# Kernel optimization log

Hardware: AMD Instinct MI355X
Metric: run time of the kernel (lower is better)

Reference implementation:

```python
import jax, jax.numpy as jnp
import numpy as np

B, T, V, C = 4, 2048, 1024, 256
NB_L, NB_M, NB_H = 16, 32, 64


def _band_w(basis, coeffs, soft):
    # basis: (V, 2*nb), coeffs: (C, 2*nb) -> w: (V, C)
    w = basis @ coeffs.T
    return jax.nn.softmax(w, axis=0) if soft else w


def _rms_norm(x):
    eps = jnp.asarray(jnp.finfo(x.dtype).eps, x.dtype)
    return x * jax.lax.rsqrt(jnp.mean(jnp.square(x), axis=-1, keepdims=True) + eps)


def _retrieve(x, basis, qc, kc, vc, decay_logit):
    # x: (B,T,V) -> (B,T,C); decay-weighted dense T x T retrieval
    q = x @ _band_w(basis, qc, True)
    k = x @ _band_w(basis, kc, True)
    v = x @ _band_w(basis, vc, True)
    scores = jnp.einsum('btc,bsc->bts', q, k)
    decay = jax.nn.sigmoid(decay_logit)
    pos = jnp.arange(T)
    diff = pos[None, :] - pos[:, None]  # diff[i,j] = j - i (as in torch code)
    dw = (decay ** jnp.maximum(diff - 1, 0).astype(x.dtype)) * (diff > 0).astype(x.dtype)
    return jnp.einsum('bts,bsc->btc', scores * dw[None], v)


def _project(r, basis, oc, out_scale):
    return jnp.einsum('btc,vc->btv', r, basis @ oc.T) * out_scale


def _transform(x, basis, read_c, mix, bias):
    z = x @ _band_w(basis, read_c, True)
    return jax.nn.gelu(z @ mix + bias, approximate=False)


def _write_back(h, basis, write_c, out_scale):
    return jnp.einsum('btc,vc->btv', h, basis @ write_c.T) * out_scale


def setup_inputs() -> dict:
    key = jax.random.key(0)
    ks = iter(jax.random.split(key, 48))
    s = 0.02

    def rn(shape, scale=s):
        return jax.random.normal(next(ks), shape, dtype=jnp.float32) * scale

    d = {
        'x': jax.random.normal(next(ks), (B, T, V), dtype=jnp.float32),
        'basis_low': jax.random.normal(next(ks), (V, 2 * NB_L), dtype=jnp.float32),
        'basis_mid': jax.random.normal(next(ks), (V, 2 * NB_M), dtype=jnp.float32),
        'basis_high': jax.random.normal(next(ks), (V, 2 * NB_H), dtype=jnp.float32),
    }
    for pre, nb, dec in (('slow', NB_L, 4.0), ('fast', NB_H, 2.0)):
        for nm in ('q', 'k', 'v', 'o'):
            d[f'{pre}_{nm}'] = rn((C, 2 * nb))
        d[f'{pre}_decay'] = jnp.asarray(dec, jnp.float32)
        d[f'{pre}_scale'] = jnp.asarray(0.1, jnp.float32)
    for pre, nb in (('low', NB_L), ('mid', NB_M), ('high', NB_H)):
        d[f'{pre}_read'] = rn((C, 2 * nb))
        d[f'{pre}_write'] = rn((C, 2 * nb))
        d[f'{pre}_mix'] = rn((C, C))
        d[f'{pre}_bias'] = jnp.zeros((C,), jnp.float32)
        d[f'{pre}_oscale'] = jnp.asarray(0.1, jnp.float32)
    d['tg_w'] = rn((C, C)); d['tg_b'] = jnp.zeros((C,), jnp.float32)
    d['alpha_w'] = rn((C, C)); d['alpha_b'] = jnp.zeros((C,), jnp.float32)
    for nm in ('mem_slow_scale', 'mem_fast_scale', 'op_low_scale', 'op_mid_scale', 'op_high_scale'):
        d[nm] = jnp.ones((1,), jnp.float32)
    return d


def reference(x, basis_low, basis_mid, basis_high,
              slow_q, slow_k, slow_v, slow_o, slow_decay, slow_scale,
              fast_q, fast_k, fast_v, fast_o, fast_decay, fast_scale,
              low_read, low_write, low_mix, low_bias, low_oscale,
              mid_read, mid_write, mid_mix, mid_bias, mid_oscale,
              high_read, high_write, high_mix, high_bias, high_oscale,
              tg_w, tg_b, alpha_w, alpha_b,
              mem_slow_scale, mem_fast_scale, op_low_scale, op_mid_scale, op_high_scale):
    # Phase 1: temporal mixing
    xn = _rms_norm(x)
    r_slow = _retrieve(xn, basis_low, slow_q, slow_k, slow_v, slow_decay)
    r_fast = _retrieve(xn, basis_high, fast_q, fast_k, fast_v, fast_decay)
    tg = jax.nn.sigmoid(r_slow @ tg_w + tg_b)
    r_fast = tg * r_fast
    x = x + (_project(r_slow, basis_low, slow_o, slow_scale) * mem_slow_scale
             + _project(r_fast, basis_high, fast_o, fast_scale) * mem_fast_scale)
    # Phase 2: band processing
    xn = _rms_norm(x)
    h_low = _transform(xn, basis_low, low_read, low_mix, low_bias)
    h_mid = _transform(xn, basis_mid, mid_read, mid_mix, mid_bias)
    h_high = _transform(xn, basis_high, high_read, high_mix, high_bias)
    ag = jax.nn.sigmoid(h_low @ alpha_w + alpha_b)
    h_high = ag * h_high
    x = x + (_write_back(h_low, basis_low, low_write, low_oscale) * op_low_scale
             + _write_back(h_mid, basis_mid, mid_write, mid_oscale) * op_mid_scale
             + _write_back(h_high, basis_high, high_write, high_oscale) * op_high_scale)
    return x
```

## Files before the change

kernel.cpp:

```cpp
#include <hip/hip_runtime.h>
#include <math.h>

#define BB 4
#define TT 2048
#define VV 1024
#define CC 256
#define MR (BB*TT)

using short8  = __attribute__((ext_vector_type(8))) short;
using ushort8 = __attribute__((ext_vector_type(8))) unsigned short;
using f32x4   = __attribute__((ext_vector_type(4))) float;

__device__ __forceinline__ float bs2f(unsigned short s) {
    return __uint_as_float(((unsigned int)s) << 16);
}
__device__ __forceinline__ unsigned short f2bs(float f) {
    unsigned int u = __float_as_uint(f);
    u += 0x7fffu + ((u >> 16) & 1u);
    return (unsigned short)(u >> 16);
}
__device__ __forceinline__ void gl_lds16(const void* g, void* l) {
    __builtin_amdgcn_global_load_lds(
        (const __attribute__((address_space(1))) unsigned int*)g,
        (__attribute__((address_space(3))) unsigned int*)l, 16, 0, 0);
}
__device__ __forceinline__ float sigm(float x) { return 1.f / (1.f + expf(-x)); }

struct CastJob { const float* src; unsigned short* dst; int n; };
struct CastArgs { CastJob j[17]; };

__global__ void cast_bf16_multi(CastArgs a) {
    CastJob jb = a.j[blockIdx.x];
    int off = (blockIdx.y * 256 + threadIdx.x) * 8;
    if (off + 8 > jb.n) return;
    float4 v0 = *reinterpret_cast<const float4*>(jb.src + off);
    float4 v1 = *reinterpret_cast<const float4*>(jb.src + off + 4);
    ushort8 u;
    u[0] = f2bs(v0.x); u[1] = f2bs(v0.y); u[2] = f2bs(v0.z); u[3] = f2bs(v0.w);
    u[4] = f2bs(v1.x); u[5] = f2bs(v1.y); u[6] = f2bs(v1.z); u[7] = f2bs(v1.w);
    *reinterpret_cast<ushort8*>(jb.dst + off) = u;
}

__global__ void softmax_rows(unsigned short* __restrict__ w) {
    int r = blockIdx.x, t = threadIdx.x;
    unsigned short* row = w + (size_t)r * 1024;
    ushort4 u = reinterpret_cast<ushort4*>(row)[t];
    float v0 = bs2f(u.x), v1 = bs2f(u.y), v2 = bs2f(u.z), v3 = bs2f(u.w);
    __shared__ float red[256];
    red[t] = fmaxf(fmaxf(v0, v1), fmaxf(v2, v3));
    __syncthreads();
    for (int o = 128; o > 0; o >>= 1) { if (t < o) red[t] = fmaxf(red[t], red[t + o]); __syncthreads(); }
    float mx = red[0]; __syncthreads();
    float e0 = expf(v0 - mx), e1 = expf(v1 - mx), e2 = expf(v2 - mx), e3 = expf(v3 - mx);
    red[t] = e0 + e1 + e2 + e3;
    __syncthreads();
    for (int o = 128; o > 0; o >>= 1) { if (t < o) red[t] += red[t + o]; __syncthreads(); }
    float inv = 1.f / red[0];
    ushort4 o4;
    o4.x = f2bs(e0 * inv); o4.y = f2bs(e1 * inv); o4.z = f2bs(e2 * inv); o4.w = f2bs(e3 * inv);
    reinterpret_cast<ushort4*>(row)[t] = o4;
}

__global__ void prep_T5(const float* s0, const float* s1, const float* s2,
                        const float* s3, const float* s4,
                        unsigned short* d0, unsigned short* d1, unsigned short* d2,
                        unsigned short* d3, unsigned short* d4) {
    int y = blockIdx.y;
    const float* W = y == 0 ? s0 : y == 1 ? s1 : y == 2 ? s2 : y == 3 ? s3 : s4;
    unsigned short* WT = y == 0 ? d0 : y == 1 ? d1 : y == 2 ? d2 : y == 3 ? d3 : d4;
    int n = blockIdx.x, k = threadIdx.x;
    WT[(size_t)n * 256 + k] = f2bs(W[(size_t)k * 256 + n]);
}

__global__ void rmsnorm_k(const float* __restrict__ x, unsigned short* __restrict__ xn) {
    int row = blockIdx.x, t = threadIdx.x;
    const float4 v = reinterpret_cast<const float4*>(x + (size_t)row * VV)[t];
    __shared__ float red[256];
    red[t] = v.x * v.x + v.y * v.y + v.z * v.z + v.w * v.w;
    __syncthreads();
    for (int o = 128; o > 0; o >>= 1) { if (t < o) red[t] += red[t + o]; __syncthreads(); }
    float r = rsqrtf(red[0] * (1.f / VV) + 1.1920929e-7f);
    ushort4 u;
    u.x = f2bs(v.x * r); u.y = f2bs(v.y * r); u.z = f2bs(v.z * r); u.w = f2bs(v.w * r);
    reinterpret_cast<ushort4*>(xn + (size_t)row * VV)[t] = u;
}

__global__ void transpose4_k(const unsigned short* __restrict__ qkv,
                             unsigned short* __restrict__ vt_s,
                             unsigned short* __restrict__ vt_f,
                             unsigned short* __restrict__ kts_s,
                             unsigned short* __restrict__ kts_f,
                             const float* __restrict__ dls,
                             const float* __restrict__ dlf) {
    __shared__ unsigned short tile[32][33];
    int z = blockIdx.z, b = z & 3, which = z >> 2;
    int srcoff = which == 0 ? 512 : which == 1 ? 1280 : which == 2 ? 256 : 1024;
    unsigned short* dst = which == 0 ? vt_s : which == 1 ? vt_f : which == 2 ? kts_s : kts_f;
    float l2d = 0.f;
    if (which == 2) l2d = log2f(sigm(dls[0]));
    if (which == 3) l2d = log2f(sigm(dlf[0]));
    int t0 = blockIdx.x * 32, c0 = blockIdx.y * 32;
    int tx = threadIdx.x & 31, ty = threadIdx.x >> 5;
    const unsigned short* src = qkv + srcoff;
    #pragma unroll
    for (int i = 0; i < 4; ++i) {
        int r = ty + i * 8;
        tile[r][tx] = src[(size_t)(b * TT + t0 + r) * 1536 + c0 + tx];
    }
    __syncthreads();
    float w = (which >= 2) ? exp2f(l2d * (float)((t0 + tx) & 127)) : 1.f;
    #pragma unroll
    for (int i = 0; i < 4; ++i) {
        int r = ty + i * 8;
        dst[((size_t)b * CC + c0 + r) * TT + t0 + tx] = f2bs(bs2f(tile[tx][r]) * w);
    }
}

__device__ __forceinline__ void gemm64_core(
    const unsigned short* A, int lda, const unsigned short* Bt, int ldb,
    int K, int m0, int n0, short8* As, short8* Bs, f32x4 (&acc)[2][2]) {
    const int tid = threadIdx.x;
    const int lane = tid & 63, wid = tid >> 6;
    const int wm = wid >> 1, wn = wid & 1;
    const int lrow = tid >> 2, lch = tid & 3;
    const int sws = lch ^ ((lrow >> 1) & 3);
    const unsigned short* ag = A + (size_t)(m0 + lrow) * lda + lch * 8;
    const unsigned short* bg = Bt + (size_t)(n0 + lrow) * ldb + lch * 8;
    #pragma unroll
    for (int i = 0; i < 2; ++i)
        #pragma unroll
        for (int j = 0; j < 2; ++j) acc[i][j] = {0.f, 0.f, 0.f, 0.f};
    const int g = lane >> 4;
    const int ra0 = wm * 32 + (lane & 15);
    const int rb0 = wn * 32 + (lane & 15);
    for (int k0 = 0; k0 < K; k0 += 32) {
        As[lrow * 4 + sws] = *reinterpret_cast<const short8*>(ag + k0);
        Bs[lrow * 4 + sws] = *reinterpret_cast<const short8*>(bg + k0);
        __syncthreads();
        short8 af[2], bf[2];
        #pragma unroll
        for (int i = 0; i < 2; ++i) {
            int ra = ra0 + i * 16;
            af[i] = As[ra * 4 + (g ^ ((ra >> 1) & 3))];
            int rb = rb0 + i * 16;
            bf[i] = Bs[rb * 4 + (g ^ ((rb >> 1) & 3))];
        }
        #pragma unroll
        for (int i = 0; i < 2; ++i)
            #pragma unroll
            for (int j = 0; j < 2; ++j)
                acc[i][j] = __builtin_amdgcn_mfma_f32_16x16x32_bf16(af[i], bf[j], acc[i][j], 0, 0, 0);
        __syncthreads();
    }
}

#define EPI_LOOP(MV, NV, VV_, BODY)                                            \
    {   const int lane_ = threadIdx.x & 63, wid_ = threadIdx.x >> 6;           \
        const int wm_ = wid_ >> 1, wn_ = wid_ & 1;                             \
        _Pragma("unroll")                                                      \
        for (int i_ = 0; i_ < 2; ++i_)                                         \
        { _Pragma("unroll")                                                    \
          for (int j_ = 0; j_ < 2; ++j_)                                       \
          { _Pragma("unroll")                                                  \
            for (int r_ = 0; r_ < 4; ++r_)                                     \
            { int MV = m0 + wm_ * 32 + i_ * 16 + (lane_ >> 4) * 4 + r_;        \
              int NV = n0 + wn_ * 32 + j_ * 16 + (lane_ & 15);                 \
              float VV_ = acc[i_][j_][r_];                                     \
              BODY } } } }

struct MJob {
    const unsigned short* A; const unsigned short* Bt; unsigned short* outb;
    const float* s1; const float* s2;
    int lda, ldb, K, ldo, gx, nblk;
};
struct MJobs5 { MJob j[5]; };

template<int EPI>
__global__ __launch_bounds__(256)
void gemm_multi_k(MJobs5 js) {
    int bid = blockIdx.x, ji = 0, base = 0;
    while (bid >= base + js.j[ji].nblk) { base += js.j[ji].nblk; ++ji; }
    MJob jb = js.j[ji];
    int rem = bid - base;
    int m0 = (rem / jb.gx) * 64, n0 = (rem % jb.gx) * 64;
    __shared__ short8 As[256], Bs[256];
    f32x4 acc[2][2];
    gemm64_core(jb.A, jb.lda, jb.Bt, jb.ldb, jb.K, m0, n0, As, Bs, acc);
    float sc = 1.f;
    if constexpr (EPI == 4) sc = jb.s1[0] * jb.s2[0];
    EPI_LOOP(m, n, v, { jb.outb[(size_t)m * jb.ldo + n] = f2bs(v * sc); })
}

__global__ __launch_bounds__(256)
void sig_k(const unsigned short* A, int lda, const unsigned short* Bt,
           const float* bias, const unsigned short* aux, int ldaux,
           unsigned short* outb, int ldo, int coloff) {
    int m0 = blockIdx.y * 64, n0 = blockIdx.x * 64;
    __shared__ short8 As[256], Bs[256];
    f32x4 acc[2][2];
    gemm64_core(A, lda, Bt, 256, 256, m0, n0, As, Bs, acc);
    EPI_LOOP(m, n, v, {
        float s = sigm(v + bias[n]);
        float a = bs2f(aux[(size_t)m * ldaux + n]);
        outb[(size_t)m * ldo + coloff + n] = f2bs(s * a);
    })
}

__global__ __launch_bounds__(256)
void gelu3_k(const unsigned short* zbuf, const unsigned short* WT_mix,
             const float* lb, const float* mb, const float* hb,
             unsigned short* hcat, unsigned short* hhigh) {
    int zi = blockIdx.z;
    const unsigned short* A = zbuf + zi * 256;
    const unsigned short* Bt = WT_mix + (size_t)zi * 65536;
    const float* bias = zi == 0 ? lb : zi == 1 ? mb : hb;
    unsigned short* outb = zi == 2 ? hhigh : hcat;
    int ldo = zi == 2 ? 256 : 768;
    int coloff = zi == 1 ? 256 : 0;
    int m0 = blockIdx.y * 64, n0 = blockIdx.x * 64;
    __shared__ short8 As[256], Bs[256];
    f32x4 acc[2][2];
    gemm64_core(A, 768, Bt, 256, 256, m0, n0, As, Bs, acc);
    EPI_LOOP(m, n, v, {
        float z = v + bias[n];
        float h = 0.5f * z * (1.f + erff(z * 0.70710678118654752f));
        outb[(size_t)m * ldo + coloff + n] = f2bs(h);
    })
}

__global__ __launch_bounds__(256)
void gstate_k(const unsigned short* kts_s, const unsigned short* vt_s,
              const unsigned short* kts_f, const unsigned short* vt_f,
              float* Gs, float* Gf) {
    int zz = blockIdx.z;
    int sel = zz >> 6, z2 = zz & 63;
    int zb = z2 >> 4, zp = z2 & 15;
    const unsigned short* A  = (sel ? kts_f : kts_s) + (size_t)(zb * CC) * TT + zp * 128;
    const unsigned short* Bt = (sel ? vt_f  : vt_s)  + (size_t)(zb * CC) * TT + zp * 128;
    float* G = (sel ? Gf : Gs) + (size_t)z2 * 65536;
    int m0 = blockIdx.y * 64, n0 = blockIdx.x * 64;
    __shared__ short8 As[256], Bs[256];
    f32x4 acc[2][2];
    gemm64_core(A, TT, Bt, TT, 128, m0, n0, As, Bs, acc);
    EPI_LOOP(m, n, v, { G[(size_t)m * 256 + n] = v; })
}

__global__ __launch_bounds__(256)
void inter_k(const unsigned short* qkv,
             const unsigned short* ST_s, const unsigned short* ST_f,
             const float* dls, const float* dlf,
             unsigned short* rcat, unsigned short* rfast) {
    int zz = blockIdx.z;
    int sel = zz >= 60, z2 = sel ? zz - 60 : zz;
    int zb = z2 / 15, zp = z2 % 15;
    const unsigned short* A = qkv + (sel ? 768 : 0) + (size_t)(zb * TT + zp * 128) * 1536;
    const unsigned short* Bt = (sel ? ST_f : ST_s) + (size_t)z2 * 65536;
    unsigned short* outb = sel ? rfast : rcat;
    int ldo = sel ? 256 : 512;
    float l2d = log2f(sigm(sel ? dlf[0] : dls[0]));
    int m0 = blockIdx.y * 64, n0 = blockIdx.x * 64;
    __shared__ short8 As[256], Bs[256];
    f32x4 acc[2][2];
    gemm64_core(A, 1536, Bt, 256, 256, m0, n0, As, Bs, acc);
    EPI_LOOP(m, n, v, {
        float rs = exp2f(l2d * (float)(127 - m));
        size_t idx = (size_t)(zb * TT + zp * 128 + m) * ldo + n;
        outb[idx] = f2bs(bs2f(outb[idx]) + v * rs);
    })
}

struct EpiP {
    float* outf; const float* addf;
    unsigned short* outb; int ldo;
};

template<int EPI>
__global__ __launch_bounds__(256)
void gemm128_k(const unsigned short* __restrict__ A, int lda,
               const unsigned short* __restrict__ Bt, int ldb, int K, EpiP ep) {
    __shared__ short8 As[1024], Bs[1024];
    const int tid = threadIdx.x;
    const int lane = tid & 63, wid = tid >> 6;
    const int wm = wid >> 1, wn = wid & 1;

    int lin = blockIdx.y * gridDim.x + blockIdx.x;
    int ngw = gridDim.x * gridDim.y;
    int q8 = ngw >> 3;
    int sw = (lin & 7) * q8 + (lin >> 3);
    const int m0 = (sw / gridDim.x) * 128, n0 = (sw % gridDim.x) * 128;

    const int srow = lane >> 3, schk = (lane & 7) ^ srow;
    const unsigned short* ga = A + (size_t)(m0 + wid * 32 + srow) * lda + schk * 8;
    const unsigned short* gb = Bt + (size_t)(n0 + wid * 32 + srow) * ldb + schk * 8;
    short8* lA = &As[(wid * 32) * 8];
    short8* lB = &Bs[(wid * 32) * 8];

    const int fr = lane & 15, fg = lane >> 4;

    f32x4 acc[4][4];
    #pragma unroll
    for (int i = 0; i < 4; ++i)
        #pragma unroll
        for (int j = 0; j < 4; ++j) acc[i][j] = {0.f, 0.f, 0.f, 0.f};

    for (int k0 = 0; k0 < K; k0 += 64) {
        #pragma unroll
        for (int q = 0; q < 4; ++q) {
            gl_lds16(ga + (size_t)(q * 8) * lda + k0, lA + q * 64);
            gl_lds16(gb + (size_t)(q * 8) * ldb + k0, lB + q * 64);
        }
        __syncthreads();
        #pragma unroll
        for (int kk = 0; kk < 2; ++kk) {
            short8 af[4], bf[4];
            #pragma unroll
            for (int i = 0; i < 4; ++i) {
                int ra = wm * 64 + i * 16 + fr;
                af[i] = As[ra * 8 + ((kk * 4 + fg) ^ (ra & 7))];
                int rb = wn * 64 + i * 16 + fr;
                bf[i] = Bs[rb * 8 + ((kk * 4 + fg) ^ (rb & 7))];
            }
            #pragma unroll
            for (int i = 0; i < 4; ++i)
                #pragma unroll
                for (int j = 0; j < 4; ++j)
                    acc[i][j] = __builtin_amdgcn_mfma_f32_16x16x32_bf16(af[i], bf[j], acc[i][j], 0, 0, 0);
        }
        __syncthreads();
    }

    #pragma unroll
    for (int i = 0; i < 4; ++i) {
        #pragma unroll
        for (int j = 0; j < 4; ++j) {
            #pragma unroll
            for (int r = 0; r < 4; ++r) {
                int m = m0 + wm * 64 + i * 16 + fg * 4 + r;
                int n = n0 + wn * 64 + j * 16 + fr;
                float v = acc[i][j][r];
                if constexpr (EPI == 0) {
                    ep.outb[(size_t)m * ep.ldo + n] = f2bs(v);
                } else {
                    size_t idx = (size_t)m * ep.ldo + n;
                    ep.outf[idx] = ep.addf[idx] + v;
                }
            }
        }
    }
}

__global__ __launch_bounds__(256)
void attn_k(const unsigned short* __restrict__ qkv,
            const unsigned short* __restrict__ vt_s,
            const unsigned short* __restrict__ vt_f,
            const float* __restrict__ dls, const float* __restrict__ dlf,
            unsigned short* __restrict__ rcat, unsigned short* __restrict__ rfast) {
    int y = blockIdx.y;
    int qoff = y ? 768 : 0, koff = y ? 1024 : 256;
    const unsigned short* vt = y ? vt_f : vt_s;
    unsigned short* rout = y ? rfast : rcat;
    int ldr = y ? 256 : 512;
    float l2d = log2f(sigm(y ? dlf[0] : dls[0]));

    int blk = blockIdx.x;
    int b = blk >> 7;
    int t0 = (blk & 127) << 4;
    int tid = threadIdx.x;
    int lane = tid & 63, wid = tid >> 6;

    __shared__ short8 Pl[4][64];
    __shared__ float  red[16][260];

    short8 qf[8];
    const size_t rowq = (size_t)(b * TT + t0 + (lane & 15)) * 1536 + qoff + (lane >> 4) * 8;
    #pragma unroll
    for (int ch = 0; ch < 8; ++ch)
        qf[ch] = *reinterpret_cast<const short8*>(qkv + rowq + ch * 32);

    f32x4 racc[16];
    #pragma unroll
    for (int i = 0; i < 16; ++i) racc[i] = {0.f, 0.f, 0.f, 0.f};

    unsigned short* pb = reinterpret_cast<unsigned short*>(&Pl[wid][0]);

    int sBeg = t0 & ~31;
    int sEnd = (t0 & ~127) + 128;
    const int tl = (lane >> 4) * 4;

    for (int s0 = sBeg + wid * 32; s0 < sEnd; s0 += 128) {
        #pragma unroll
        for (int h = 0; h < 2; ++h) {
            f32x4 sacc = {0.f, 0.f, 0.f, 0.f};
            const unsigned short* kb =
                qkv + (size_t)(b * TT + s0 + h * 16 + (lane & 15)) * 1536 + koff + (lane >> 4) * 8;
            #pragma unroll
            for (int ch = 0; ch < 8; ++ch) {
                short8 kf = *reinterpret_cast<const short8*>(kb + ch * 32);
                sacc = __builtin_amdgcn_mfma_f32_16x16x32_bf16(qf[ch], kf, sacc, 0, 0, 0);
            }
            int scol = s0 + h * 16 + (lane & 15);
            #pragma unroll
            for (int r = 0; r < 4; ++r) {
                int trow = t0 + tl + r;
                int d = scol - trow;
                float w = (d > 0) ? exp2f(l2d * (float)(d - 1)) : 0.f;
                int prow = tl + r, pcol = h * 16 + (lane & 15);
                int swp = (pcol >> 3) ^ ((prow >> 1) & 3);
                pb[(prow * 4 + swp) * 8 + (pcol & 7)] = f2bs(sacc[r] * w);
            }
        }
        asm volatile("s_waitcnt lgkmcnt(0)" ::: "memory");
        __builtin_amdgcn_sched_barrier(0);
        short8 pf;
        { int prow = lane & 15; pf = Pl[wid][prow * 4 + ((lane >> 4) ^ ((prow >> 1) & 3))]; }
        const unsigned short* vb = vt + ((size_t)b * CC + (lane & 15)) * TT + s0 + (lane >> 4) * 8;
        #pragma unroll
        for (int nt = 0; nt < 16; ++nt) {
            short8 vf = *reinterpret_cast<const short8*>(vb + (size_t)nt * 16 * TT);
            racc[nt] = __builtin_amdgcn_mfma_f32_16x16x32_bf16(pf, vf, racc[nt], 0, 0, 0);
        }
    }

    for (int w = 0; w < 4; ++w) {
        if (wid == w) {
            #pragma unroll
            for (int nt = 0; nt < 16; ++nt)
                #pragma unroll
                for (int r = 0; r < 4; ++r) {
                    int row = tl + r, col = nt * 16 + (lane & 15);
                    if (w == 0) red[row][col] = racc[nt][r];
                    else        red[row][col] += racc[nt][r];
                }
        }
        __syncthreads();
    }

    {
        int row = tid >> 4, c0 = (tid & 15) * 16;
        ushort8 lo, hi;
        #pragma unroll
        for (int j = 0; j < 8; ++j) lo[j] = f2bs(red[row][c0 + j]);
        #pragma unroll
        for (int j = 0; j < 8; ++j) hi[j] = f2bs(red[row][c0 + 8 + j]);
        unsigned short* dst = rout + (size_t)(b * TT + t0 + row) * ldr + c0;
        *reinterpret_cast<ushort8*>(dst)     = lo;
        *reinterpret_cast<ushort8*>(dst + 8) = hi;
    }
}

__global__ void scan_states(const float* __restrict__ G,
                            const float* __restrict__ dlogit,
                            unsigned short* __restrict__ ST) {
    int b = blockIdx.y;
    int e0 = (blockIdx.x * 256 + threadIdx.x) * 4;
    float d = sigm(dlogit[0]);
    float dL = exp2f(log2f(d) * 128.f);
    float4 s = {0.f, 0.f, 0.f, 0.f};
    int i = e0 >> 8, j0 = e0 & 255;
    for (int c = 15; c >= 1; --c) {
        float4 g = *reinterpret_cast<const float4*>(G + (((size_t)(b * 16 + c)) << 16) + e0);
        s.x = g.x + dL * s.x; s.y = g.y + dL * s.y;
        s.z = g.z + dL * s.z; s.w = g.w + dL * s.w;
        unsigned short* dst = ST + (((size_t)(b * 15 + c - 1)) << 16);
        dst[(j0 + 0) * 256 + i] = f2bs(s.x);
        dst[(j0 + 1) * 256 + i] = f2bs(s.y);
        dst[(j0 + 2) * 256 + i] = f2bs(s.z);
        dst[(j0 + 3) * 256 + i] = f2bs(s.w);
    }
}

extern "C" void kernel_launch(void* const* d_in, const int* in_sizes, int n_in,
                              void* d_out, int out_size, void* d_ws, size_t ws_size,
                              hipStream_t stream) {
    (void)in_sizes; (void)n_in; (void)out_size; (void)ws_size;
    const float* x          = (const float*)d_in[0];
    const float* basis_low  = (const float*)d_in[1];
    const float* basis_mid  = (const float*)d_in[2];
    const float* basis_high = (const float*)d_in[3];
    const float* slow_q = (const float*)d_in[4];
    const float* slow_k = (const float*)d_in[5];
    const float* slow_v = (const float*)d_in[6];
    const float* slow_o = (const float*)d_in[7];
    const float* slow_decay = (const float*)d_in[8];
    const float* slow_scale = (const float*)d_in[9];
    const float* fast_q = (const float*)d_in[10];
    const float* fast_k = (const float*)d_in[11];
    const float* fast_v = (const float*)d_in[12];
    const float* fast_o = (const float*)d_in[13];
    const float* fast_decay = (const float*)d_in[14];
    const float* fast_scale = (const float*)d_in[15];
    const float* low_read  = (const float*)d_in[16];
    const float* low_write = (const float*)d_in[17];
    const float* low_mix   = (const float*)d_in[18];
    const float* low_bias  = (const float*)d_in[19];
    const float* low_oscale= (const float*)d_in[20];
    const float* mid_read  = (const float*)d_in[21];
    const float* mid_write = (const float*)d_in[22];
    const float* mid_mix   = (const float*)d_in[23];
    const float* mid_bias  = (const float*)d_in[24];
    const float* mid_oscale= (const float*)d_in[25];
    const float* high_read  = (const float*)d_in[26];
    const float* high_write = (const float*)d_in[27];
    const float* high_mix   = (const float*)d_in[28];
    const float* high_bias  = (const float*)d_in[29];
    const float* high_oscale= (const float*)d_in[30];
    const float* tg_w    = (const float*)d_in[31];
    const float* tg_b    = (const float*)d_in[32];
    const float* alpha_w = (const float*)d_in[33];
    const float* alpha_b = (const float*)d_in[34];
    const float* mem_slow_scale = (const float*)d_in[35];
    const float* mem_fast_scale = (const float*)d_in[36];
    const float* op_low_scale   = (const float*)d_in[37];
    const float* op_mid_scale   = (const float*)d_in[38];
    const float* op_high_scale  = (const float*)d_in[39];
    float* out = (float*)d_out;

    char* ws = (char*)d_ws;
    size_t off = 0;
    auto alloc = [&](size_t n) { char* p = ws + off; off += (n + 255) & ~(size_t)255; return p; };
    unsigned short* WT_p1   = (unsigned short*)alloc((size_t)6 * CC * VV * 2);
    unsigned short* WT_read = (unsigned short*)alloc((size_t)3 * CC * VV * 2);
    unsigned short* Wcat_o  = (unsigned short*)alloc((size_t)VV * 512 * 2);
    unsigned short* Wcat_w  = (unsigned short*)alloc((size_t)VV * 768 * 2);
    unsigned short* WT_mix  = (unsigned short*)alloc((size_t)3 * 65536 * 2);
    unsigned short* WT_tg   = (unsigned short*)alloc((size_t)65536 * 2);
    unsigned short* WT_al   = (unsigned short*)alloc((size_t)65536 * 2);
    unsigned short* bb_low  = (unsigned short*)alloc((size_t)VV * 32 * 2);
    unsigned short* bb_mid  = (unsigned short*)alloc((size_t)VV * 64 * 2);
    unsigned short* bb_high = (unsigned short*)alloc((size_t)VV * 128 * 2);
    unsigned short* cqkv_l  = (unsigned short*)alloc((size_t)768 * 32 * 2);
    unsigned short* cqkv_h  = (unsigned short*)alloc((size_t)768 * 128 * 2);
    unsigned short* crd_l   = (unsigned short*)alloc((size_t)256 * 32 * 2);
    unsigned short* crd_m   = (unsigned short*)alloc((size_t)256 * 64 * 2);
    unsigned short* crd_h   = (unsigned short*)alloc((size_t)256 * 128 * 2);
    unsigned short* cO_s    = (unsigned short*)alloc((size_t)256 * 32 * 2);
    unsigned short* cO_f    = (unsigned short*)alloc((size_t)256 * 128 * 2);
    unsigned short* cW_l    = (unsigned short*)alloc((size_t)256 * 32 * 2);
    unsigned short* cW_m    = (unsigned short*)alloc((size_t)256 * 64 * 2);
    unsigned short* cW_h    = (unsigned short*)alloc((size_t)256 * 128 * 2);
    unsigned short* xn      = (unsigned short*)alloc((size_t)MR * VV * 2);
    unsigned short* qkv     = (unsigned short*)alloc((size_t)MR * 1536 * 2);
    unsigned short* vt_s    = (unsigned short*)alloc((size_t)BB * CC * TT * 2);
    unsigned short* vt_f    = (unsigned short*)alloc((size_t)BB * CC * TT * 2);
    unsigned short* kts_s   = (unsigned short*)alloc((size_t)BB * CC * TT * 2);
    unsigned short* kts_f   = (unsigned short*)alloc((size_t)BB * CC * TT * 2);
    unsigned short* ST_s    = (unsigned short*)alloc((size_t)BB * 15 * 65536 * 2);
    unsigned short* ST_f    = (unsigned short*)alloc((size_t)BB * 15 * 65536 * 2);
    unsigned short* rcat    = (unsigned short*)alloc((size_t)MR * 512 * 2);
    unsigned short* rfast   = (unsigned short*)alloc((size_t)MR * CC * 2);
    unsigned short* hhigh   = (unsigned short*)alloc((size_t)MR * CC * 2);
    float* Gs = (float*)xn;
    float* Gf = (float*)rcat;
    unsigned short* z    = qkv;
    unsigned short* hcat = qkv + (size_t)MR * 768;

    {
        CastArgs ca;
        int i = 0;
        auto J = [&](const float* s, unsigned short* d, int n) { ca.j[i].src = s; ca.j[i].dst = d; ca.j[i].n = n; ++i; };
        J(basis_low,  bb_low,  VV * 32);
        J(basis_mid,  bb_mid,  VV * 64);
        J(basis_high, bb_high, VV * 128);
        J(slow_q, cqkv_l + 0 * 256 * 32, 256 * 32);
        J(slow_k, cqkv_l + 1 * 256 * 32, 256 * 32);
        J(slow_v, cqkv_l + 2 * 256 * 32, 256 * 32);
        J(fast_q, cqkv_h + 0 * 256 * 128, 256 * 128);
        J(fast_k, cqkv_h + 1 * 256 * 128, 256 * 128);
        J(fast_v, cqkv_h + 2 * 256 * 128, 256 * 128);
        J(low_read,  crd_l, 256 * 32);
        J(mid_read,  crd_m, 256 * 64);
        J(high_read, crd_h, 256 * 128);
        J(slow_o,    cO_s,  256 * 32);
        J(fast_o,    cO_f,  256 * 128);
        J(low_write, cW_l,  256 * 32);
        J(mid_write, cW_m,  256 * 64);
        J(high_write,cW_h,  256 * 128);
        cast_bf16_multi<<<dim3(17, 64), 256, 0, stream>>>(ca);
    }

    {
        MJobs5 js;
        auto S = [&](int i, const unsigned short* A, int lda, const unsigned short* B, int K,
                     unsigned short* o, int nb) {
            js.j[i].A = A; js.j[i].Bt = B; js.j[i].outb = o; js.j[i].s1 = nullptr; js.j[i].s2 = nullptr;
            js.j[i].lda = lda; js.j[i].ldb = K; js.j[i].K = K; js.j[i].ldo = VV; js.j[i].gx = 16; js.j[i].nblk = nb;
        };
        S(0, cqkv_l, 32,  bb_low,  32,  WT_p1,                    192);
        S(1, cqkv_h, 128, bb_high, 128, WT_p1 + (size_t)768 * VV, 192);
        S(2, crd_l,  32,  bb_low,  32,  WT_read,                   64);
        S(3, crd_m,  64,  bb_mid,  64,  WT_read + (size_t)256 * VV, 64);
        S(4, crd_h,  128, bb_high, 128, WT_read + (size_t)512 * VV, 64);
        gemm_multi_k<0><<<576, 256, 0, stream>>>(js);
    }
    softmax_rows<<<2304, 256, 0, stream>>>(WT_p1);

    {
        MJobs5 js;
        auto S = [&](int i, const unsigned short* A, int lda, const unsigned short* B, int K,
                     unsigned short* o, int ldo, const float* s1, const float* s2) {
            js.j[i].A = A; js.j[i].Bt = B; js.j[i].outb = o; js.j[i].s1 = s1; js.j[i].s2 = s2;
            js.j[i].lda = lda; js.j[i].ldb = K; js.j[i].K = K; js.j[i].ldo = ldo; js.j[i].gx = 4; js.j[i].nblk = 64;
        };
        S(0, bb_low,  32,  cO_s, 32,  Wcat_o,       512, slow_scale,  mem_slow_scale);
        S(1, bb_high, 128, cO_f, 128, Wcat_o + 256, 512, fast_scale,  mem_fast_scale);
        S(2, bb_low,  32,  cW_l, 32,  Wcat_w,       768, low_oscale,  op_low_scale);
        S(3, bb_mid,  64,  cW_m, 64,  Wcat_w + 256, 768, mid_oscale,  op_mid_scale);
        S(4, bb_high, 128, cW_h, 128, Wcat_w + 512, 768, high_oscale, op_high_scale);
        gemm_multi_k<4><<<320, 256, 0, stream>>>(js);
    }

    prep_T5<<<dim3(256, 5), 256, 0, stream>>>(tg_w, alpha_w, low_mix, mid_mix, high_mix,
                                              WT_tg, WT_al, WT_mix, WT_mix + 65536, WT_mix + 131072);

    rmsnorm_k<<<MR, 256, 0, stream>>>(x, xn);
    { EpiP ep{}; ep.outb = qkv; ep.ldo = 1536;
      gemm128_k<0><<<dim3(12, 64), 256, 0, stream>>>(xn, 1024, WT_p1, 1024, 1024, ep); }
    transpose4_k<<<dim3(64, 8, 16), 256, 0, stream>>>(qkv, vt_s, vt_f, kts_s, kts_f, slow_decay, fast_decay);
    gstate_k<<<dim3(4, 4, 128), 256, 0, stream>>>(kts_s, vt_s, kts_f, vt_f, Gs, Gf);
    scan_states<<<dim3(64, 4), 256, 0, stream>>>(Gs, slow_decay, ST_s);
    scan_states<<<dim3(64, 4), 256, 0, stream>>>(Gf, fast_decay, ST_f);
    attn_k<<<dim3(512, 2), 256, 0, stream>>>(qkv, vt_s, vt_f, slow_decay, fast_decay, rcat, rfast);
    inter_k<<<dim3(4, 2, 120), 256, 0, stream>>>(qkv, ST_s, ST_f, slow_decay, fast_decay, rcat, rfast);
    sig_k<<<dim3(4, 128), 256, 0, stream>>>(rcat, 512, WT_tg, tg_b, rfast, 256, rcat, 512, 256);
    { EpiP ep{}; ep.outf = out; ep.addf = x; ep.ldo = 1024;
      gemm128_k<3><<<dim3(8, 64), 256, 0, stream>>>(rcat, 512, Wcat_o, 512, 512, ep); }

    rmsnorm_k<<<MR, 256, 0, stream>>>(out, xn);
    { EpiP ep{}; ep.outb = z; ep.ldo = 768;
      gemm128_k<0><<<dim3(6, 64), 256, 0, stream>>>(xn, 1024, WT_read, 1024, 1024, ep); }
    gelu3_k<<<dim3(4, 128, 3), 256, 0, stream>>>(z, WT_mix, low_bias, mid_bias, high_bias, hcat, hhigh);
    sig_k<<<dim3(4, 128), 256, 0, stream>>>(hcat, 768, WT_al, alpha_b, hhigh, 256, hcat, 768, 512);
    { EpiP ep{}; ep.outf = out; ep.addf = out; ep.ldo = 1024;
      gemm128_k<3><<<dim3(6, 64), 256, 0, stream>>>(hcat, 768, Wcat_w, 768, 768, ep); }
}
```

Baseline: 315.3 us.

## Double-buffer LDS in gemm128_k and merge the two scan_states launches

The 128x128 GEMM kernel now keeps two LDS buffers and issues the global-to-LDS loads for the next K tile before computing the current one. It waits with explicit vmcnt counts and raw s_barrier instead of a full __syncthreads, so load latency can overlap MFMA work. The two scan_states launches for the slow and fast paths are merged into one launch using blockIdx.z, saving one kernel launch. The GEMM doubles its LDS footprint, which may lower occupancy, and its correctness depends on the hand-written waitcnt matching the eight outstanding loads per stage.

```diff
diff --git a/kernel.cpp b/kernel.cpp
--- a/kernel.cpp
+++ b/kernel.cpp
@@ -278,7 +278,7 @@
 __global__ __launch_bounds__(256)
 void gemm128_k(const unsigned short* __restrict__ A, int lda,
                const unsigned short* __restrict__ Bt, int ldb, int K, EpiP ep) {
-    __shared__ short8 As[1024], Bs[1024];
+    __shared__ short8 As[2][1024], Bs[2][1024];
     const int tid = threadIdx.x;
     const int lane = tid & 63, wid = tid >> 6;
     const int wm = wid >> 1, wn = wid & 1;
@@ -292,8 +292,6 @@
     const int srow = lane >> 3, schk = (lane & 7) ^ srow;
     const unsigned short* ga = A + (size_t)(m0 + wid * 32 + srow) * lda + schk * 8;
     const unsigned short* gb = Bt + (size_t)(n0 + wid * 32 + srow) * ldb + schk * 8;
-    short8* lA = &As[(wid * 32) * 8];
-    short8* lB = &Bs[(wid * 32) * 8];
 
     const int fr = lane & 15, fg = lane >> 4;
 
@@ -303,22 +301,36 @@
         #pragma unroll
         for (int j = 0; j < 4; ++j) acc[i][j] = {0.f, 0.f, 0.f, 0.f};
 
-    for (int k0 = 0; k0 < K; k0 += 64) {
+    auto stage = [&](int buf, int k0) {
+        short8* lA = &As[buf][(wid * 32) * 8];
+        short8* lB = &Bs[buf][(wid * 32) * 8];
         #pragma unroll
         for (int q = 0; q < 4; ++q) {
             gl_lds16(ga + (size_t)(q * 8) * lda + k0, lA + q * 64);
             gl_lds16(gb + (size_t)(q * 8) * ldb + k0, lB + q * 64);
         }
-        __syncthreads();
+    };
+
+    stage(0, 0);
+    int cur = 0;
+    for (int k0 = 0; k0 < K; k0 += 64) {
+        if (k0 + 64 < K) {
+            stage(cur ^ 1, k0 + 64);
+            asm volatile("s_waitcnt vmcnt(8)" ::: "memory");
+        } else {
+            asm volatile("s_waitcnt vmcnt(0)" ::: "memory");
+        }
+        __builtin_amdgcn_s_barrier();
+        __builtin_amdgcn_sched_barrier(0);
         #pragma unroll
         for (int kk = 0; kk < 2; ++kk) {
             short8 af[4], bf[4];
             #pragma unroll
             for (int i = 0; i < 4; ++i) {
                 int ra = wm * 64 + i * 16 + fr;
-                af[i] = As[ra * 8 + ((kk * 4 + fg) ^ (ra & 7))];
+                af[i] = As[cur][ra * 8 + ((kk * 4 + fg) ^ (ra & 7))];
                 int rb = wn * 64 + i * 16 + fr;
-                bf[i] = Bs[rb * 8 + ((kk * 4 + fg) ^ (rb & 7))];
+                bf[i] = Bs[cur][rb * 8 + ((kk * 4 + fg) ^ (rb & 7))];
             }
             #pragma unroll
             for (int i = 0; i < 4; ++i)
@@ -326,7 +338,9 @@
                 for (int j = 0; j < 4; ++j)
                     acc[i][j] = __builtin_amdgcn_mfma_f32_16x16x32_bf16(af[i], bf[j], acc[i][j], 0, 0, 0);
         }
-        __syncthreads();
+        __builtin_amdgcn_sched_barrier(0);
+        __builtin_amdgcn_s_barrier();
+        cur ^= 1;
     }
 
     #pragma unroll
@@ -448,12 +462,15 @@
     }
 }
 
-__global__ void scan_states(const float* __restrict__ G,
-                            const float* __restrict__ dlogit,
-                            unsigned short* __restrict__ ST) {
+__global__ void scan_states2(const float* __restrict__ Gs, const float* __restrict__ Gf,
+                             const float* __restrict__ dls, const float* __restrict__ dlf,
+                             unsigned short* __restrict__ STs, unsigned short* __restrict__ STf) {
+    int sel = blockIdx.z;
+    const float* G = sel ? Gf : Gs;
+    unsigned short* ST = sel ? STf : STs;
+    float d = sigm(sel ? dlf[0] : dls[0]);
     int b = blockIdx.y;
     int e0 = (blockIdx.x * 256 + threadIdx.x) * 4;
-    float d = sigm(dlogit[0]);
     float dL = exp2f(log2f(d) * 128.f);
     float4 s = {0.f, 0.f, 0.f, 0.f};
     int i = e0 >> 8, j0 = e0 & 255;
@@ -617,8 +634,7 @@
       gemm128_k<0><<<dim3(12, 64), 256, 0, stream>>>(xn, 1024, WT_p1, 1024, 1024, ep); }
     transpose4_k<<<dim3(64, 8, 16), 256, 0, stream>>>(qkv, vt_s, vt_f, kts_s, kts_f, slow_decay, fast_decay);
     gstate_k<<<dim3(4, 4, 128), 256, 0, stream>>>(kts_s, vt_s, kts_f, vt_f, Gs, Gf);
-    scan_states<<<dim3(64, 4), 256, 0, stream>>>(Gs, slow_decay, ST_s);
-    scan_states<<<dim3(64, 4), 256, 0, stream>>>(Gf, fast_decay, ST_f);
+    scan_states2<<<dim3(64, 4, 2), 256, 0, stream>>>(Gs, Gf, slow_decay, fast_decay, ST_s, ST_f);
     attn_k<<<dim3(512, 2), 256, 0, stream>>>(qkv, vt_s, vt_f, slow_decay, fast_decay, rcat, rfast);
     inter_k<<<dim3(4, 2, 120), 256, 0, stream>>>(qkv, ST_s, ST_f, slow_decay, fast_decay, rcat, rfast);
     sig_k<<<dim3(4, 128), 256, 0, stream>>>(rcat, 512, WT_tg, tg_b, rfast, 256, rcat, 512, 256);
```

New measurement: 327.3 us. 1.04x slower.
